# Kernel tuning notes

Measured on AMD Instinct MI355X. Metric: run time of the kernel, lower is better.

## Reference

```python
import jax, jax.numpy as jnp
import numpy as np

B = 32768
F = 256
H1 = 16
H2 = 8

def setup_inputs() -> dict:
    key = jax.random.key(0)
    ks = jax.random.split(key, 9)
    x = jax.random.normal(ks[0], (B, F), dtype=jnp.float32)
    # Stacked per-feature MLP params (one UnivariateNetwork per feature)
    W1 = jax.random.normal(ks[1], (F, H1), dtype=jnp.float32) * (1.0 / np.sqrt(1))
    b1 = jax.random.normal(ks[2], (F, H1), dtype=jnp.float32) * 0.05
    W2 = jax.random.normal(ks[3], (F, H1, H2), dtype=jnp.float32) * (1.0 / np.sqrt(H1))
    b2 = jax.random.normal(ks[4], (F, H2), dtype=jnp.float32) * 0.05
    W3 = jax.random.normal(ks[5], (F, H2), dtype=jnp.float32) * (1.0 / np.sqrt(H2))
    b3 = jax.random.normal(ks[6], (F,), dtype=jnp.float32) * 0.05
    theta = jax.random.uniform(ks[7], (F,), dtype=jnp.float32) * 0.05
    bias = jnp.zeros((1,), dtype=jnp.float32)
    return {"x": x, "W1": W1, "b1": b1, "W2": W2, "b2": b2,
            "W3": W3, "b3": b3, "theta": theta, "bias": bias}

def reference(x, W1, b1, W2, b2, W3, b3, theta, bias):
    # Batched per-feature MLP: 1 -> H1 -> H2 -> 1 with ELU, all features at once.
    h1 = jax.nn.elu(x[:, :, None] * W1[None, :, :] + b1[None, :, :])      # [B, F, H1]
    h2 = jax.nn.elu(jnp.einsum('bfh,fhk->bfk', h1, W2) + b2[None, :, :])  # [B, F, H2]
    Z = jnp.einsum('bfk,fk->bf', h2, W3) + b3[None, :]                    # [B, F]
    weights = jax.nn.softplus(theta)                                      # [F]
    y_pred = Z @ weights + bias                                           # [B]
    return (y_pred, weights, Z)
```

## Files before the change

### kernel.cpp

```cpp
#include <hip/hip_runtime.h>

#define NB 32768
#define NF 256
#define H1 16
#define H2 8
#define ROWS_PER_BLOCK 1024
#define ITERS (ROWS_PER_BLOCK / 64)
#define FPB 4
#define NT (FPB * 64)

__device__ __forceinline__ float elu_f(float v) {
    return v > 0.0f ? v : (__expf(v) - 1.0f);
}
__device__ __forceinline__ float rfl(float v) {
    return __int_as_float(__builtin_amdgcn_readfirstlane(__float_as_int(v)));
}

__global__ __launch_bounds__(NT, 5)
void z_kernel(const float* __restrict__ x,  const float* __restrict__ W1,
              const float* __restrict__ b1, const float* __restrict__ W2,
              const float* __restrict__ b2, const float* __restrict__ W3,
              const float* __restrict__ b3, float* __restrict__ z_out) {
    const int wave = threadIdx.x >> 6;
    const int lane = threadIdx.x & 63;
    const int f    = blockIdx.y * FPB + wave;
    const int rowBase = blockIdx.x * ROWS_PER_BLOCK;

    __shared__ float lds_w2[FPB][64];

    if (lane < 16) {
        const float4 v = reinterpret_cast<const float4*>(W2 + f * H1 * H2 + 64)[lane];
        reinterpret_cast<float4*>(lds_w2[wave])[lane] = v;
    }

    float s_w2[8 * H2];
    {
        const float4* p = reinterpret_cast<const float4*>(W2 + f * H1 * H2);
        #pragma unroll
        for (int i = 0; i < 16; ++i) {
            float4 v = p[i];
            s_w2[4*i]   = rfl(v.x); s_w2[4*i+1] = rfl(v.y);
            s_w2[4*i+2] = rfl(v.z); s_w2[4*i+3] = rfl(v.w);
        }
    }
    float w1v[H1], s_b1[H1];
    {
        const float4* pw = reinterpret_cast<const float4*>(W1 + f * H1);
        const float4* pb = reinterpret_cast<const float4*>(b1 + f * H1);
        #pragma unroll
        for (int i = 0; i < 4; ++i) {
            float4 v = pw[i];
            w1v[4*i] = v.x; w1v[4*i+1] = v.y; w1v[4*i+2] = v.z; w1v[4*i+3] = v.w;
        }
        #pragma unroll
        for (int i = 0; i < 4; ++i) {
            float4 v = pb[i];
            s_b1[4*i]   = rfl(v.x); s_b1[4*i+1] = rfl(v.y);
            s_b1[4*i+2] = rfl(v.z); s_b1[4*i+3] = rfl(v.w);
        }
    }
    float b2v[H2];
    {
        const float4* p = reinterpret_cast<const float4*>(b2 + f * H2);
        float4 v0 = p[0], v1 = p[1];
        b2v[0]=v0.x; b2v[1]=v0.y; b2v[2]=v0.z; b2v[3]=v0.w;
        b2v[4]=v1.x; b2v[5]=v1.y; b2v[6]=v1.z; b2v[7]=v1.w;
    }
    float s_w3[H2];
    {
        const float4* p = reinterpret_cast<const float4*>(W3 + f * H2);
        float4 v0 = p[0], v1 = p[1];
        s_w3[0]=rfl(v0.x); s_w3[1]=rfl(v0.y); s_w3[2]=rfl(v0.z); s_w3[3]=rfl(v0.w);
        s_w3[4]=rfl(v1.x); s_w3[5]=rfl(v1.y); s_w3[6]=rfl(v1.z); s_w3[7]=rfl(v1.w);
    }
    const float s_b3 = rfl(b3[f]);

    __syncthreads();

    const float* wbase = lds_w2[wave];

    const int off0 = (rowBase + lane) * NF + f;
    float h1c[H1];
    {
        const float xv = x[off0];
        #pragma unroll
        for (int h = 0; h < H1; ++h)
            h1c[h] = elu_f(fmaf(xv, w1v[h], s_b1[h]));
    }
    float xn  = x[off0 + 64 * NF];
    int off = off0;

    #pragma unroll 1
    for (int it = 0; it < ITERS; ++it) {
        const int off2 = off + 2 * 64 * NF;
        const float xnn = x[(it + 2 < ITERS) ? off2 : off];

        float acc[H2];
        #pragma unroll
        for (int k = 0; k < H2; ++k) acc[k] = b2v[k];

        #pragma unroll
        for (int h = 0; h < 8; ++h) {
            const float hc = h1c[h];
            h1c[h] = elu_f(fmaf(xn, w1v[h], s_b1[h]));
            #pragma unroll
            for (int k = 0; k < H2; ++k)
                acc[k] = fmaf(hc, s_w2[h * H2 + k], acc[k]);
        }

        int dsoff = 0;
        asm volatile("" : "+v"(dsoff));
        const float4* wp = reinterpret_cast<const float4*>(wbase + dsoff);
        #pragma unroll
        for (int h = 0; h < 8; ++h) {
            const float4 wlo = wp[2 * h];
            const float4 whi = wp[2 * h + 1];
            const float hc = h1c[8 + h];
            h1c[8 + h] = elu_f(fmaf(xn, w1v[8 + h], s_b1[8 + h]));
            acc[0] = fmaf(hc, wlo.x, acc[0]);
            acc[1] = fmaf(hc, wlo.y, acc[1]);
            acc[2] = fmaf(hc, wlo.z, acc[2]);
            acc[3] = fmaf(hc, wlo.w, acc[3]);
            acc[4] = fmaf(hc, whi.x, acc[4]);
            acc[5] = fmaf(hc, whi.y, acc[5]);
            acc[6] = fmaf(hc, whi.z, acc[6]);
            acc[7] = fmaf(hc, whi.w, acc[7]);
        }

        float z = s_b3;
        #pragma unroll
        for (int k = 0; k < H2; ++k)
            z = fmaf(elu_f(acc[k]), s_w3[k], z);

        z_out[off] = z;
        off += 64 * NF; xn = xnn;
    }
}

#define NT2 256
#define ROWS2 64
__global__ __launch_bounds__(NT2, 4)
void y_kernel(const float* __restrict__ z, const float* __restrict__ theta,
              const float* __restrict__ bias, float* __restrict__ y_out,
              float* __restrict__ w_out) {
    __shared__ __align__(16) float wls[NF];
    const int tid = threadIdx.x;
    {
        const float th = theta[tid];
        const float w  = logf(1.0f + __expf(th));
        wls[tid] = w;
        if (blockIdx.x == 0) w_out[tid] = w;
    }
    __syncthreads();
    const int wave = tid >> 6, lane = tid & 63;
    const float4 w4 = reinterpret_cast<const float4*>(wls)[lane];
    const float biasv = bias[0];
    #pragma unroll 1
    for (int r = 0; r < ROWS2 / 4; ++r) {
        const int row = blockIdx.x * ROWS2 + wave * (ROWS2 / 4) + r;
        const float4 zv = reinterpret_cast<const float4*>(z + row * NF)[lane];
        float s = zv.x * w4.x + zv.y * w4.y + zv.z * w4.z + zv.w * w4.w;
        #pragma unroll
        for (int o = 32; o > 0; o >>= 1) s += __shfl_down(s, o, 64);
        if (lane == 0) y_out[row] = s + biasv;
    }
}

extern "C" void kernel_launch(void* const* d_in, const int* in_sizes, int n_in,
                              void* d_out, int out_size, void* d_ws, size_t ws_size,
                              hipStream_t stream) {
    const float* x     = (const float*)d_in[0];
    const float* W1    = (const float*)d_in[1];
    const float* b1    = (const float*)d_in[2];
    const float* W2    = (const float*)d_in[3];
    const float* b2    = (const float*)d_in[4];
    const float* W3    = (const float*)d_in[5];
    const float* b3    = (const float*)d_in[6];
    const float* theta = (const float*)d_in[7];
    const float* bias  = (const float*)d_in[8];

    float* y_out = (float*)d_out;
    float* w_out = y_out + NB;
    float* z_out = w_out + NF;

    dim3 grid1(NB / ROWS_PER_BLOCK, NF / FPB);
    z_kernel<<<grid1, NT, 0, stream>>>(x, W1, b1, W2, b2, W3, b3, z_out);
    y_kernel<<<NB / ROWS2, NT2, 0, stream>>>(z_out, theta, bias, y_out, w_out);
}
```

Measured before the change: 162.4 us.

## Fuse y reduction into z kernel via atomics and use packed FMAs

Removes the separate y kernel. Each feature wave now computes softplus(theta[f]) itself and atomically adds w·z, plus the bias once per row, into y_out, which is zeroed by an async memset beforehand. This avoids re-reading the full Z matrix and a second launch, at the cost of many global float atomics per row and a nondeterministic summation order. The second-layer accumulators are also regrouped into 2-wide float vectors so the compiler can emit packed FMA instructions for the LDS-weight half.

Result: slower. 184.8 us (+13.8%).

```diff
diff --git a/kernel.cpp b/kernel.cpp
--- a/kernel.cpp
+++ b/kernel.cpp
@@ -8,6 +8,8 @@
 #define ITERS (ROWS_PER_BLOCK / 64)
 #define FPB 4
 #define NT (FPB * 64)
+
+typedef float v2f __attribute__((ext_vector_type(2)));
 
 __device__ __forceinline__ float elu_f(float v) {
     return v > 0.0f ? v : (__expf(v) - 1.0f);
@@ -20,7 +22,10 @@
 void z_kernel(const float* __restrict__ x,  const float* __restrict__ W1,
               const float* __restrict__ b1, const float* __restrict__ W2,
               const float* __restrict__ b2, const float* __restrict__ W3,
-              const float* __restrict__ b3, float* __restrict__ z_out) {
+              const float* __restrict__ b3, const float* __restrict__ theta,
+              const float* __restrict__ bias,
+              float* __restrict__ y_out, float* __restrict__ w_out,
+              float* __restrict__ z_out) {
     const int wave = threadIdx.x >> 6;
     const int lane = threadIdx.x & 63;
     const int f    = blockIdx.y * FPB + wave;
@@ -59,12 +64,12 @@
             s_b1[4*i+2] = rfl(v.z); s_b1[4*i+3] = rfl(v.w);
         }
     }
-    float b2v[H2];
+    v2f b2p[4];
     {
         const float4* p = reinterpret_cast<const float4*>(b2 + f * H2);
         float4 v0 = p[0], v1 = p[1];
-        b2v[0]=v0.x; b2v[1]=v0.y; b2v[2]=v0.z; b2v[3]=v0.w;
-        b2v[4]=v1.x; b2v[5]=v1.y; b2v[6]=v1.z; b2v[7]=v1.w;
+        b2p[0] = (v2f){v0.x, v0.y}; b2p[1] = (v2f){v0.z, v0.w};
+        b2p[2] = (v2f){v1.x, v1.y}; b2p[3] = (v2f){v1.z, v1.w};
     }
     float s_w3[H2];
     {
@@ -74,6 +79,10 @@
         s_w3[4]=rfl(v1.x); s_w3[5]=rfl(v1.y); s_w3[6]=rfl(v1.z); s_w3[7]=rfl(v1.w);
     }
     const float s_b3 = rfl(b3[f]);
+    const float wv = rfl(logf(1.0f + __expf(theta[f])));
+    const float ybias = (blockIdx.y == 0 && wave == 0) ? bias[0] : 0.0f;
+
+    if (blockIdx.x == 0 && lane == 0) w_out[f] = wv;
 
     __syncthreads();
 
@@ -95,17 +104,22 @@
         const int off2 = off + 2 * 64 * NF;
         const float xnn = x[(it + 2 < ITERS) ? off2 : off];
 
-        float acc[H2];
+        v2f accp[4];
         #pragma unroll
-        for (int k = 0; k < H2; ++k) acc[k] = b2v[k];
+        for (int j = 0; j < 4; ++j) accp[j] = b2p[j];
 
         #pragma unroll
         for (int h = 0; h < 8; ++h) {
             const float hc = h1c[h];
             h1c[h] = elu_f(fmaf(xn, w1v[h], s_b1[h]));
-            #pragma unroll
-            for (int k = 0; k < H2; ++k)
-                acc[k] = fmaf(hc, s_w2[h * H2 + k], acc[k]);
+            accp[0].x = fmaf(hc, s_w2[h*H2 + 0], accp[0].x);
+            accp[0].y = fmaf(hc, s_w2[h*H2 + 1], accp[0].y);
+            accp[1].x = fmaf(hc, s_w2[h*H2 + 2], accp[1].x);
+            accp[1].y = fmaf(hc, s_w2[h*H2 + 3], accp[1].y);
+            accp[2].x = fmaf(hc, s_w2[h*H2 + 4], accp[2].x);
+            accp[2].y = fmaf(hc, s_w2[h*H2 + 5], accp[2].y);
+            accp[3].x = fmaf(hc, s_w2[h*H2 + 6], accp[3].x);
+            accp[3].y = fmaf(hc, s_w2[h*H2 + 7], accp[3].y);
         }
 
         int dsoff = 0;
@@ -117,52 +131,24 @@
             const float4 whi = wp[2 * h + 1];
             const float hc = h1c[8 + h];
             h1c[8 + h] = elu_f(fmaf(xn, w1v[8 + h], s_b1[8 + h]));
-            acc[0] = fmaf(hc, wlo.x, acc[0]);
-            acc[1] = fmaf(hc, wlo.y, acc[1]);
-            acc[2] = fmaf(hc, wlo.z, acc[2]);
-            acc[3] = fmaf(hc, wlo.w, acc[3]);
-            acc[4] = fmaf(hc, whi.x, acc[4]);
-            acc[5] = fmaf(hc, whi.y, acc[5]);
-            acc[6] = fmaf(hc, whi.z, acc[6]);
-            acc[7] = fmaf(hc, whi.w, acc[7]);
+            const v2f hcp = (v2f){hc, hc};
+            accp[0] += (v2f){wlo.x, wlo.y} * hcp;
+            accp[1] += (v2f){wlo.z, wlo.w} * hcp;
+            accp[2] += (v2f){whi.x, whi.y} * hcp;
+            accp[3] += (v2f){whi.z, whi.w} * hcp;
         }
 
         float z = s_b3;
         #pragma unroll
-        for (int k = 0; k < H2; ++k)
-            z = fmaf(elu_f(acc[k]), s_w3[k], z);
+        for (int j = 0; j < 4; ++j) {
+            z = fmaf(elu_f(accp[j].x), s_w3[2*j],     z);
+            z = fmaf(elu_f(accp[j].y), s_w3[2*j + 1], z);
+        }
 
         z_out[off] = z;
+        atomicAdd(y_out + (rowBase + it * 64 + lane), fmaf(wv, z, ybias));
+
         off += 64 * NF; xn = xnn;
-    }
-}
-
-#define NT2 256
-#define ROWS2 64
-__global__ __launch_bounds__(NT2, 4)
-void y_kernel(const float* __restrict__ z, const float* __restrict__ theta,
-              const float* __restrict__ bias, float* __restrict__ y_out,
-              float* __restrict__ w_out) {
-    __shared__ __align__(16) float wls[NF];
-    const int tid = threadIdx.x;
-    {
-        const float th = theta[tid];
-        const float w  = logf(1.0f + __expf(th));
-        wls[tid] = w;
-        if (blockIdx.x == 0) w_out[tid] = w;
-    }
-    __syncthreads();
-    const int wave = tid >> 6, lane = tid & 63;
-    const float4 w4 = reinterpret_cast<const float4*>(wls)[lane];
-    const float biasv = bias[0];
-    #pragma unroll 1
-    for (int r = 0; r < ROWS2 / 4; ++r) {
-        const int row = blockIdx.x * ROWS2 + wave * (ROWS2 / 4) + r;
-        const float4 zv = reinterpret_cast<const float4*>(z + row * NF)[lane];
-        float s = zv.x * w4.x + zv.y * w4.y + zv.z * w4.z + zv.w * w4.w;
-        #pragma unroll
-        for (int o = 32; o > 0; o >>= 1) s += __shfl_down(s, o, 64);
-        if (lane == 0) y_out[row] = s + biasv;
     }
 }
 
@@ -183,7 +169,9 @@
     float* w_out = y_out + NB;
     float* z_out = w_out + NF;
 
+    hipMemsetAsync(y_out, 0, NB * sizeof(float), stream);
+
     dim3 grid1(NB / ROWS_PER_BLOCK, NF / FPB);
-    z_kernel<<<grid1, NT, 0, stream>>>(x, W1, b1, W2, b2, W3, b3, z_out);
-    y_kernel<<<NB / ROWS2, NT2, 0, stream>>>(z_out, theta, bias, y_out, w_out);
+    z_kernel<<<grid1, NT, 0, stream>>>(x, W1, b1, W2, b2, W3, b3, theta, bias,
+                                       y_out, w_out, z_out);
 }
```
